# Optimization experiments

Measured on AMD Instinct MI355X. Metric: run time of the kernel, lower is better.

The kernel has to match this reference:

```python
import jax, jax.numpy as jnp
import numpy as np

B, S, D = 4, 2048, 1024
H = 16
DH = D // H  # attention_head_size = 64


def setup_inputs() -> dict:
    key = jax.random.key(0)
    ks = jax.random.split(key, 7)
    scale = 0.02
    return {
        "hidden_states": jax.random.normal(ks[0], (B, S, D), dtype=jnp.float32),
        "Wq": jax.random.normal(ks[1], (D, D), dtype=jnp.float32) * scale,
        "bq": jnp.zeros((D,), dtype=jnp.float32),
        "Wk": jax.random.normal(ks[2], (D, D), dtype=jnp.float32) * scale,
        "bk": jnp.zeros((D,), dtype=jnp.float32),
        "Wv": jax.random.normal(ks[3], (D, D), dtype=jnp.float32) * scale,
        "bv": jnp.zeros((D,), dtype=jnp.float32),
    }


def _split_heads(x):
    # [B, S, D] -> [B, H, S, DH]
    b, s, _ = x.shape
    return x.reshape(b, s, H, DH).transpose(0, 2, 1, 3)


def reference(hidden_states, Wq, bq, Wk, bk, Wv, bv):
    # torch nn.Linear computes x @ W.T + b
    q = _split_heads(hidden_states @ Wq.T + bq)  # [B,H,S,DH]
    k = _split_heads(hidden_states @ Wk.T + bk)
    v = _split_heads(hidden_states @ Wv.T + bv)

    scores = jnp.einsum("bhqd,bhkd->bhqk", q, k) / jnp.sqrt(jnp.float32(DH))
    # original detaches attention probs (LRP-style)
    probs = jax.lax.stop_gradient(jax.nn.softmax(scores, axis=-1))
    ctx = jnp.einsum("bhqk,bhkd->bhqd", probs, v)  # [B,H,S,DH]
    # [B,H,S,DH] -> [B,S,D]
    return ctx.transpose(0, 2, 1, 3).reshape(hidden_states.shape[0], hidden_states.shape[1], D)
```

## Files before the change

kernel.cpp:

```cpp
#include <hip/hip_runtime.h>

typedef _Float16 f16;
typedef f16 f16x2 __attribute__((ext_vector_type(2)));
typedef f16 f16x4 __attribute__((ext_vector_type(4)));
typedef f16 f16x8 __attribute__((ext_vector_type(8)));
typedef float f32x4 __attribute__((ext_vector_type(4)));

#define NB 4
#define NS 2048
#define ND 1024
#define NH 16
#define NDH 64

__device__ __forceinline__ void gl2lds16(const void* g, void* l) {
  __builtin_amdgcn_global_load_lds(
      (const __attribute__((address_space(1))) unsigned int*)g,
      (__attribute__((address_space(3))) unsigned int*)l, 16, 0, 0);
}

__device__ __forceinline__ float fast_exp2(float x) {
  return __builtin_amdgcn_exp2f(x);
}

__device__ __forceinline__ f16x2 pk_f16(float a, float b) {
  return __builtin_bit_cast(f16x2, __builtin_amdgcn_cvt_pkrtz(a, b));
}

__global__ __launch_bounds__(256) void cvt_all(
    const float* __restrict__ X, const float* __restrict__ Wq,
    const float* __restrict__ Wk, const float* __restrict__ Wv,
    f16* __restrict__ Xh, f16* __restrict__ Wh) {
  int b = blockIdx.x;
  const float* src;
  f16* dst;
  int off;
  if (b < 8192)       { src = X;  dst = Xh;               off = 0; }
  else if (b < 9216)  { src = Wq; dst = Wh;               off = 8192; }
  else if (b < 10240) { src = Wk; dst = Wh + (1u << 20);  off = 9216; }
  else                { src = Wv; dst = Wh + (2u << 20);  off = 10240; }
  int i = (b - off) * 256 + threadIdx.x;
  float4 v = ((const float4*)src)[i];
  f16x4 h = {(f16)v.x, (f16)v.y, (f16)v.z, (f16)v.w};
  ((f16x4*)dst)[i] = h;
}

__global__ __launch_bounds__(256) void qkv_gemm(
    const f16* __restrict__ Xh, const f16* __restrict__ Wh,
    const float* __restrict__ bq, const float* __restrict__ bk,
    const float* __restrict__ bv,
    f16* __restrict__ QF, f16* __restrict__ KF, f16* __restrict__ VF) {
  __shared__ f16 Ah[128 * 64];
  __shared__ f16 Bh[128 * 64];
  const int t = threadIdx.x;
  const int tileM = blockIdx.x * 128;
  const int nGlob = blockIdx.y * 128;
  const int mat = nGlob >> 10;
  const int col0 = nGlob & 1023;
  const int wave = t >> 6, lane = t & 63;
  const int mOff = (wave & 1) * 64, nOff = (wave >> 1) * 64;
  const int lr = lane & 15, quad = lane >> 4;

  f32x4 acc[4][4];
#pragma unroll
  for (int i = 0; i < 4; i++)
#pragma unroll
    for (int j = 0; j < 4; j++) acc[i][j] = f32x4{0.f, 0.f, 0.f, 0.f};

  const int srow = t >> 3;
  const int sx = ((t & 7) ^ (srow & 7)) * 8;
  const f16* ag = Xh + (size_t)(tileM + srow) * ND + sx;
  const f16* bg = Wh + (size_t)mat * ND * ND + (size_t)(col0 + srow) * ND + sx;
  const bool qk = (mat < 2);
  const int rx = lr & 7;

  for (int kk = 0; kk < ND; kk += 64) {
    __syncthreads();
    gl2lds16(ag + kk,                       Ah + t * 8);
    gl2lds16(ag + (size_t)32 * ND + kk,     Ah + 2048 + t * 8);
    gl2lds16(ag + (size_t)64 * ND + kk,     Ah + 4096 + t * 8);
    gl2lds16(ag + (size_t)96 * ND + kk,     Ah + 6144 + t * 8);
    gl2lds16(bg + kk,                       Bh + t * 8);
    gl2lds16(bg + (size_t)32 * ND + kk,     Bh + 2048 + t * 8);
    gl2lds16(bg + (size_t)64 * ND + kk,     Bh + 4096 + t * 8);
    gl2lds16(bg + (size_t)96 * ND + kk,     Bh + 6144 + t * 8);
    __syncthreads();
#pragma unroll
    for (int c = 0; c < 2; c++) {
      const int ch = ((c * 4 + quad) ^ rx) * 8;
      f16x8 af[4], bf[4];
#pragma unroll
      for (int i = 0; i < 4; i++)
        af[i] = *(const f16x8*)(Ah + (mOff + i * 16 + lr) * 64 + ch);
#pragma unroll
      for (int j = 0; j < 4; j++)
        bf[j] = *(const f16x8*)(Bh + (nOff + j * 16 + lr) * 64 + ch);
      if (qk) {
#pragma unroll
        for (int i = 0; i < 4; i++)
#pragma unroll
          for (int j = 0; j < 4; j++)
            acc[i][j] = __builtin_amdgcn_mfma_f32_16x16x32_f16(bf[j], af[i], acc[i][j], 0, 0, 0);
      } else {
#pragma unroll
        for (int i = 0; i < 4; i++)
#pragma unroll
          for (int j = 0; j < 4; j++)
            acc[i][j] = __builtin_amdgcn_mfma_f32_16x16x32_f16(af[i], bf[j], acc[i][j], 0, 0, 0);
      }
    }
  }

  if (qk) {
    const float* bias = (mat == 0) ? bq : bk;
    f16* dst = (mat == 0) ? QF : KF;
    const float sc = (mat == 0) ? 0.18033688f : 1.0f;
    const int jstart = (quad & 1) * 4;
#pragma unroll
    for (int j = 0; j < 4; j++) {
      int n0 = col0 + nOff + j * 16;
      int h = n0 >> 6;
      int f = j >> 1;
      int lam = lr + 16 * ((2 * j + (quad >> 1)) & 3);
      float4 bb = *(const float4*)(bias + n0 + quad * 4);
#pragma unroll
      for (int i = 0; i < 4; i++) {
        int sF = tileM + mOff + i * 16;
        int b = sF >> 11, st = (sF & 2047) >> 4;
        int bh = b * NH + h;
        f16x4 v;
#pragma unroll
        for (int r = 0; r < 4; r++) v[r] = (f16)((acc[i][j][r] + (&bb.x)[r]) * sc);
        *(f16x4*)(dst + (((size_t)(bh * 128 + st) * 2 + f) * 64 + lam) * 8 + jstart) = v;
      }
    }
  } else {
#pragma unroll
    for (int j = 0; j < 4; j++) {
      int n = col0 + nOff + j * 16 + lr;
      int h = n >> 6, dt = (n >> 4) & 3;
      float bb = bv[n];
#pragma unroll
      for (int i = 0; i < 4; i++) {
        int sF = tileM + mOff + i * 16;
        int b = sF >> 11;
        int kt2 = (sF & 2047) >> 5;
        int ts = (sF >> 4) & 1;
        int bh = b * NH + h;
        f16x4 v;
#pragma unroll
        for (int r = 0; r < 4; r++) v[r] = (f16)(acc[i][j][r] + bb);
        *(f16x4*)(VF + ((size_t)(bh * 64 + kt2) * 4 + dt) * 512 +
                  (size_t)(quad * 16 + lr) * 8 + 4 * ts) = v;
      }
    }
  }
}

__global__ __launch_bounds__(512, 4) void attn_kernel(
    const f16* __restrict__ QF, const f16* __restrict__ KF,
    const f16* __restrict__ VF, float* __restrict__ out) {
  const int t = threadIdx.x, wave = t >> 6, lane = t & 63;
  const int lr = lane & 15, quad = lane >> 4;
  const int bh = blockIdx.x, qb = blockIdx.y;
  const int bb = bh >> 4, hh = bh & 15;
  const size_t bhOff = (size_t)bh * 131072;
  const f16* Qp = QF + bhOff + (size_t)lane * 8;
  const f16* Kp = KF + bhOff + (size_t)lane * 8;
  const f16* Vp = VF + bhOff + (size_t)lane * 8;
  const int st0 = qb * 16 + wave * 2;

  f16x8 qf[2][2];
#pragma unroll
  for (int qt = 0; qt < 2; qt++) {
    qf[qt][0] = *(const f16x8*)(Qp + (size_t)(st0 + qt) * 1024);
    qf[qt][1] = *(const f16x8*)(Qp + (size_t)(st0 + qt) * 1024 + 512);
  }

  f32x4 o[2][4];
#pragma unroll
  for (int qt = 0; qt < 2; qt++)
#pragma unroll
    for (int dt = 0; dt < 4; dt++) o[qt][dt] = f32x4{0.f, 0.f, 0.f, 0.f};
  f32x4 lacc[2];
#pragma unroll
  for (int qt = 0; qt < 2; qt++) lacc[qt] = f32x4{0.f, 0.f, 0.f, 0.f};
  const f16x8 ones8 = {(f16)1.f, (f16)1.f, (f16)1.f, (f16)1.f,
                       (f16)1.f, (f16)1.f, (f16)1.f, (f16)1.f};

  f16x8 kk[4], vv[4];
#pragma unroll
  for (int i = 0; i < 4; i++) kk[i] = *(const f16x8*)(Kp + i * 512);
#pragma unroll
  for (int i = 0; i < 4; i++) vv[i] = *(const f16x8*)(Vp + i * 512);

  for (int kt2 = 0; kt2 < 64; ++kt2) {
    f32x4 sA[2], sB[2];
#pragma unroll
    for (int qt = 0; qt < 2; qt++) {
      sA[qt] = f32x4{0.f, 0.f, 0.f, 0.f};
      sA[qt] = __builtin_amdgcn_mfma_f32_16x16x32_f16(kk[0], qf[qt][0], sA[qt], 0, 0, 0);
      sA[qt] = __builtin_amdgcn_mfma_f32_16x16x32_f16(kk[1], qf[qt][1], sA[qt], 0, 0, 0);
      sB[qt] = f32x4{0.f, 0.f, 0.f, 0.f};
      sB[qt] = __builtin_amdgcn_mfma_f32_16x16x32_f16(kk[2], qf[qt][0], sB[qt], 0, 0, 0);
      sB[qt] = __builtin_amdgcn_mfma_f32_16x16x32_f16(kk[3], qf[qt][1], sB[qt], 0, 0, 0);
    }
    const size_t nk = (size_t)((kt2 + 1) & 63) * 2048;
    f16x8 nkk[4];
#pragma unroll
    for (int i = 0; i < 4; i++) nkk[i] = *(const f16x8*)(Kp + nk + i * 512);
    f16x8 pf[2];
#pragma unroll
    for (int qt = 0; qt < 2; qt++) {
      f16x2 a0 = pk_f16(fast_exp2(sA[qt][0]), fast_exp2(sA[qt][1]));
      f16x2 a1 = pk_f16(fast_exp2(sA[qt][2]), fast_exp2(sA[qt][3]));
      f16x2 b0 = pk_f16(fast_exp2(sB[qt][0]), fast_exp2(sB[qt][1]));
      f16x2 b1 = pk_f16(fast_exp2(sB[qt][2]), fast_exp2(sB[qt][3]));
      f16x4 lo = __builtin_shufflevector(a0, a1, 0, 1, 2, 3);
      f16x4 hi = __builtin_shufflevector(b0, b1, 0, 1, 2, 3);
      pf[qt] = __builtin_shufflevector(lo, hi, 0, 1, 2, 3, 4, 5, 6, 7);
    }
#pragma unroll
    for (int dt = 0; dt < 4; dt++)
#pragma unroll
      for (int qt = 0; qt < 2; qt++)
        o[qt][dt] = __builtin_amdgcn_mfma_f32_16x16x32_f16(pf[qt], vv[dt], o[qt][dt], 0, 0, 0);
#pragma unroll
    for (int qt = 0; qt < 2; qt++)
      lacc[qt] = __builtin_amdgcn_mfma_f32_16x16x32_f16(pf[qt], ones8, lacc[qt], 0, 0, 0);
    f16x8 nvv[4];
#pragma unroll
    for (int i = 0; i < 4; i++) nvv[i] = *(const f16x8*)(Vp + nk + i * 512);
#pragma unroll
    for (int i = 0; i < 4; i++) { kk[i] = nkk[i]; vv[i] = nvv[i]; }
  }

#pragma unroll
  for (int qt = 0; qt < 2; qt++) {
#pragma unroll
    for (int r = 0; r < 4; r++) {
      float inv = 1.0f / lacc[qt][r];
      int q = qb * 256 + wave * 32 + qt * 16 + quad * 4 + r;
#pragma unroll
      for (int dt = 0; dt < 4; dt++)
        out[((size_t)bb * NS + q) * ND + hh * 64 + dt * 16 + lr] = o[qt][dt][r] * inv;
    }
  }
}

extern "C" void kernel_launch(void* const* d_in, const int* in_sizes, int n_in,
                              void* d_out, int out_size, void* d_ws, size_t ws_size,
                              hipStream_t stream) {
  const float* X  = (const float*)d_in[0];
  const float* Wq = (const float*)d_in[1];
  const float* bq = (const float*)d_in[2];
  const float* Wk = (const float*)d_in[3];
  const float* bk = (const float*)d_in[4];
  const float* Wv = (const float*)d_in[5];
  const float* bv = (const float*)d_in[6];
  float* out = (float*)d_out;

  f16* Xh = (f16*)d_ws;
  f16* Wh = (f16*)((char*)d_ws + (size_t)(16u << 20));
  f16* QF = (f16*)((char*)d_ws + (size_t)(22u << 20));
  f16* KF = (f16*)((char*)d_ws + (size_t)(38u << 20));
  f16* VF = (f16*)((char*)d_ws + (size_t)(54u << 20));

  cvt_all<<<11264, 256, 0, stream>>>(X, Wq, Wk, Wv, Xh, Wh);
  qkv_gemm<<<dim3(64, 24), 256, 0, stream>>>(Xh, Wh, bq, bk, bv, QF, KF, VF);
  attn_kernel<<<dim3(64, 8), 512, 0, stream>>>(QF, KF, VF, out);
}
```

Before: 225.4 us.

## Stage K/V tiles through double-buffered LDS with async global-to-LDS loads

Each block cooperatively loads the next K/V tile into a double-buffered shared-memory buffer with global_load_lds, and every wave then reads K/V from LDS. Previously each of the 8 waves loaded the full K/V tile from global memory into registers on its own. The goal is to cut redundant global/L2 traffic and register pressure. In exchange it adds a __syncthreads per iteration and LDS reads, which may stall MFMA issue because each tile is small (64 iterations).

```diff
diff --git a/kernel.cpp b/kernel.cpp
--- a/kernel.cpp
+++ b/kernel.cpp
@@ -159,15 +159,18 @@
 __global__ __launch_bounds__(512, 4) void attn_kernel(
     const f16* __restrict__ QF, const f16* __restrict__ KF,
     const f16* __restrict__ VF, float* __restrict__ out) {
+  __shared__ f16 LK[2][2048];
+  __shared__ f16 LV[2][2048];
   const int t = threadIdx.x, wave = t >> 6, lane = t & 63;
   const int lr = lane & 15, quad = lane >> 4;
   const int bh = blockIdx.x, qb = blockIdx.y;
   const int bb = bh >> 4, hh = bh & 15;
   const size_t bhOff = (size_t)bh * 131072;
   const f16* Qp = QF + bhOff + (size_t)lane * 8;
-  const f16* Kp = KF + bhOff + (size_t)lane * 8;
-  const f16* Vp = VF + bhOff + (size_t)lane * 8;
   const int st0 = qb * 16 + wave * 2;
+
+  const int sidx = t & 255;
+  const f16* sg = ((t < 256) ? KF : VF) + bhOff + (size_t)sidx * 8;
 
   f16x8 qf[2][2];
 #pragma unroll
@@ -187,13 +190,25 @@
   const f16x8 ones8 = {(f16)1.f, (f16)1.f, (f16)1.f, (f16)1.f,
                        (f16)1.f, (f16)1.f, (f16)1.f, (f16)1.f};
 
-  f16x8 kk[4], vv[4];
-#pragma unroll
-  for (int i = 0; i < 4; i++) kk[i] = *(const f16x8*)(Kp + i * 512);
-#pragma unroll
-  for (int i = 0; i < 4; i++) vv[i] = *(const f16x8*)(Vp + i * 512);
+  {
+    f16* dst = (t < 256) ? &LK[0][sidx * 8] : &LV[0][sidx * 8];
+    gl2lds16(sg, dst);
+  }
+  __syncthreads();
 
   for (int kt2 = 0; kt2 < 64; ++kt2) {
+    const int buf = kt2 & 1;
+    if (kt2 < 63) {
+      f16* dst = (t < 256) ? &LK[buf ^ 1][sidx * 8] : &LV[buf ^ 1][sidx * 8];
+      gl2lds16(sg + (size_t)(kt2 + 1) * 2048, dst);
+    }
+    f16x8 kk[4], vv[4];
+#pragma unroll
+    for (int i = 0; i < 4; i++)
+      kk[i] = *(const f16x8*)(&LK[buf][i * 512 + lane * 8]);
+#pragma unroll
+    for (int i = 0; i < 4; i++)
+      vv[i] = *(const f16x8*)(&LV[buf][i * 512 + lane * 8]);
     f32x4 sA[2], sB[2];
 #pragma unroll
     for (int qt = 0; qt < 2; qt++) {
@@ -204,10 +219,6 @@
       sB[qt] = __builtin_amdgcn_mfma_f32_16x16x32_f16(kk[2], qf[qt][0], sB[qt], 0, 0, 0);
       sB[qt] = __builtin_amdgcn_mfma_f32_16x16x32_f16(kk[3], qf[qt][1], sB[qt], 0, 0, 0);
     }
-    const size_t nk = (size_t)((kt2 + 1) & 63) * 2048;
-    f16x8 nkk[4];
-#pragma unroll
-    for (int i = 0; i < 4; i++) nkk[i] = *(const f16x8*)(Kp + nk + i * 512);
     f16x8 pf[2];
 #pragma unroll
     for (int qt = 0; qt < 2; qt++) {
@@ -227,11 +238,7 @@
 #pragma unroll
     for (int qt = 0; qt < 2; qt++)
       lacc[qt] = __builtin_amdgcn_mfma_f32_16x16x32_f16(pf[qt], ones8, lacc[qt], 0, 0, 0);
-    f16x8 nvv[4];
-#pragma unroll
-    for (int i = 0; i < 4; i++) nvv[i] = *(const f16x8*)(Vp + nk + i * 512);
-#pragma unroll
-    for (int i = 0; i < 4; i++) { kk[i] = nkk[i]; vv[i] = nvv[i]; }
+    __syncthreads();
   }
 
 #pragma unroll
```

Result: faster. 218.2 us (-3.2%).
